# Performance work log

Measured on AMD Instinct MI355X. Metric: run time of the kernel, lower is better.

Reference implementation:

```python
import jax, jax.numpy as jnp
import numpy as np

B, P, D, K, OUT = 16, 2048, 64, 16, 128


def setup_inputs() -> dict:
    key = jax.random.key(0)
    k1, k2, k3 = jax.random.split(key, 3)
    x = jax.random.normal(k1, (B * P, D), dtype=jnp.float32)
    pos = jax.random.normal(k2, (B * P, 3), dtype=jnp.float32)
    batch = jnp.repeat(jnp.arange(B, dtype=jnp.int64), P)  # sorted segment ids
    # Linear(2*D -> OUT), torch convention W: [out, in]
    W = jax.random.normal(k3, (OUT, 2 * D), dtype=jnp.float32) / np.sqrt(2 * D)
    b = jnp.zeros((OUT,), dtype=jnp.float32)
    return {"x": x, "pos": pos, "batch": batch, "W": W, "b": b}


def _knn_idx(xb):
    # xb: [P, D] one cloud; returns [P, K] indices of K nearest neighbors (self excluded)
    sq = jnp.sum(xb * xb, axis=-1)  # [P]
    d2 = sq[:, None] + sq[None, :] - 2.0 * (xb @ xb.T)  # [P, P]
    d2 = d2 + jnp.eye(P, dtype=xb.dtype) * jnp.asarray(1e10, xb.dtype)  # loop=False
    _, idx = jax.lax.top_k(-d2, K)  # smallest distances
    return idx


def reference(x, pos, batch, W, b):
    # batch is uniform segments of size P (sorted), so reshape is equivalent
    xb = x.reshape(B, P, D)
    idx = jax.vmap(_knn_idx)(xb)  # [B, P, K]
    # gather neighbor features per cloud
    xj = jax.vmap(lambda f, i: f[i])(xb, idx)  # [B, P, K, D]
    xi = jnp.broadcast_to(xb[:, :, None, :], (B, P, K, D))
    e = jnp.concatenate([xi, xj - xi], axis=-1)  # [B, P, K, 2D]
    h = jnp.einsum('bpkd,od->bpko', e, W) + b  # edge MLP
    out = jnp.max(h, axis=2)  # max aggregation over neighbors -> [B, P, OUT]
    out = jax.nn.relu(out)
    return out.reshape(B * P, OUT)
```

## Files before the change

### kernel.cpp

```cpp
#include <hip/hip_runtime.h>

typedef __bf16 bf16x8 __attribute__((ext_vector_type(8)));
typedef float  f32x4  __attribute__((ext_vector_type(4)));

#define NBAT 16
#define NP   2048
#define ND   64
#define NOUT 128
#define NK   16
#define RT   16
#define HSTR 2052

static __device__ __forceinline__ unsigned short f2bf(float f) {
    unsigned u = __float_as_uint(f);
    u += 0x7FFF + ((u >> 16) & 1);
    return (unsigned short)(u >> 16);
}
static __device__ __forceinline__ int lanes_below(unsigned long long m) {
    return (int)__builtin_amdgcn_mbcnt_hi((unsigned)(m >> 32),
             __builtin_amdgcn_mbcnt_lo((unsigned)m, 0u));
}
static __device__ __forceinline__ unsigned long long umin64(unsigned long long a, unsigned long long b){ return a < b ? a : b; }
static __device__ __forceinline__ unsigned long long umax64(unsigned long long a, unsigned long long b){ return a < b ? b : a; }

static __device__ __forceinline__ void bitonic_sort128_u64(unsigned long long &k0,
                                                           unsigned long long &k1, int lane) {
#pragma unroll
    for (int k = 2; k <= 64; k <<= 1) {
#pragma unroll
        for (int j = k >> 1; j >= 1; j >>= 1) {
            bool lower = ((lane & j) == 0);
            bool up0 = (k == 64) ? true  : ((lane & k) == 0);
            bool up1 = (k == 64) ? false : ((lane & k) == 0);
            unsigned long long o0 = __shfl_xor(k0, j, 64);
            k0 = (up0 == lower) ? umin64(k0, o0) : umax64(k0, o0);
            unsigned long long o1 = __shfl_xor(k1, j, 64);
            k1 = (up1 == lower) ? umin64(k1, o1) : umax64(k1, o1);
        }
    }
    { unsigned long long mn = umin64(k0, k1), mx = umax64(k0, k1); k0 = mn; k1 = mx; }
#pragma unroll
    for (int j = 32; j >= 1; j >>= 1) {
        bool lower = ((lane & j) == 0);
        unsigned long long o0 = __shfl_xor(k0, j, 64);
        k0 = lower ? umin64(k0, o0) : umax64(k0, o0);
        unsigned long long o1 = __shfl_xor(k1, j, 64);
        k1 = lower ? umin64(k1, o1) : umax64(k1, o1);
    }
}

static __device__ __forceinline__ float
refine_d(const float* __restrict__ x, int gr, int gcbase, int jc) {
    const float* xr = x + (size_t)gr * ND;
    const float* xc = x + (size_t)(gcbase + jc) * ND;
    double s0 = 0.0, s1 = 0.0;
#pragma unroll
    for (int k8 = 0; k8 < 8; ++k8) {
        float4 a = *(const float4*)(xr + k8 * 8);
        float4 b = *(const float4*)(xc + k8 * 8);
        float4 a2 = *(const float4*)(xr + k8 * 8 + 4);
        float4 b2 = *(const float4*)(xc + k8 * 8 + 4);
        double e0 = (double)a.x - (double)b.x;
        double e1 = (double)a.y - (double)b.y;
        double e2 = (double)a.z - (double)b.z;
        double e3 = (double)a.w - (double)b.w;
        s0 = fma(e0, e0, s0); s0 = fma(e1, e1, s0);
        s0 = fma(e2, e2, s0); s0 = fma(e3, e3, s0);
        double f0 = (double)a2.x - (double)b2.x;
        double f1 = (double)a2.y - (double)b2.y;
        double f2 = (double)a2.z - (double)b2.z;
        double f3 = (double)a2.w - (double)b2.w;
        s1 = fma(f0, f0, s1); s1 = fma(f1, f1, s1);
        s1 = fma(f2, f2, s1); s1 = fma(f3, f3, s1);
    }
    return (float)(s0 + s1);
}

static __device__ __forceinline__ void cvt_hilo(const float* __restrict__ p,
                                                bf16x8 &hi, bf16x8 &lo) {
    float4 a = *(const float4*)p, b = *(const float4*)(p + 4);
    float f[8] = {a.x, a.y, a.z, a.w, b.x, b.y, b.z, b.w};
#pragma unroll
    for (int i = 0; i < 8; ++i) {
        __bf16 h = (__bf16)f[i];
        hi[i] = h;
        lo[i] = (__bf16)(f[i] - (float)h);
    }
}

__global__ void __launch_bounds__(256)
prep_k(const float* __restrict__ x,
       const float* __restrict__ W,
       const float* __restrict__ bias,
       float* __restrict__ sq, float* __restrict__ U,
       float* __restrict__ V,  unsigned short* __restrict__ xb16)
{
    const int blk = blockIdx.x, tid = threadIdx.x;
    const int R0 = blk * 16;
    const int w  = tid >> 6, l = tid & 63;
    const int l15 = l & 15, lg = l >> 4, kc = lg * 8;

    {
        int r = tid >> 4, c = (tid & 15) * 4;
        float4 v = *(const float4*)(x + (size_t)(R0 + r) * ND + c);
        ushort4 hb;
        hb.x = f2bf(v.x); hb.y = f2bf(v.y); hb.z = f2bf(v.z); hb.w = f2bf(v.w);
        *(ushort4*)(xb16 + (size_t)(R0 + r) * ND + c) = hb;
    }
    if (tid < 128) {
        int r = tid >> 3, seg = tid & 7;
        const float* p = x + (size_t)(R0 + r) * ND + seg * 8;
        float4 a = *(const float4*)(p);
        float4 b = *(const float4*)(p + 4);
        double s = (double)a.x * a.x + (double)a.y * a.y +
                   (double)a.z * a.z + (double)a.w * a.w +
                   (double)b.x * b.x + (double)b.y * b.y +
                   (double)b.z * b.z + (double)b.w * b.w;
        s += __shfl_xor(s, 1, 64);
        s += __shfl_xor(s, 2, 64);
        s += __shfl_xor(s, 4, 64);
        if (seg == 0) sq[R0 + r] = (float)s;
    }

    const float* xr = x + (size_t)(R0 + l15) * ND + kc;
    bf16x8 bh0, bl0, bh1, bl1;
    cvt_hilo(xr,      bh0, bl0);
    cvt_hilo(xr + 32, bh1, bl1);

#pragma unroll
    for (int tt = 0; tt < 2; ++tt) {
        const int ot = w + tt * 4;
        const float* wb = W + (size_t)(ot * 16 + l15) * (2 * ND) + kc;
        f32x4 accP = {0.f, 0.f, 0.f, 0.f};
        f32x4 accV = {0.f, 0.f, 0.f, 0.f};
        bf16x8 ah, al;
        cvt_hilo(wb, ah, al);
        accP = __builtin_amdgcn_mfma_f32_16x16x32_bf16(ah, bh0, accP, 0, 0, 0);
        accP = __builtin_amdgcn_mfma_f32_16x16x32_bf16(ah, bl0, accP, 0, 0, 0);
        accP = __builtin_amdgcn_mfma_f32_16x16x32_bf16(al, bh0, accP, 0, 0, 0);
        cvt_hilo(wb + 32, ah, al);
        accP = __builtin_amdgcn_mfma_f32_16x16x32_bf16(ah, bh1, accP, 0, 0, 0);
        accP = __builtin_amdgcn_mfma_f32_16x16x32_bf16(ah, bl1, accP, 0, 0, 0);
        accP = __builtin_amdgcn_mfma_f32_16x16x32_bf16(al, bh1, accP, 0, 0, 0);
        cvt_hilo(wb + 64, ah, al);
        accV = __builtin_amdgcn_mfma_f32_16x16x32_bf16(ah, bh0, accV, 0, 0, 0);
        accV = __builtin_amdgcn_mfma_f32_16x16x32_bf16(ah, bl0, accV, 0, 0, 0);
        accV = __builtin_amdgcn_mfma_f32_16x16x32_bf16(al, bh0, accV, 0, 0, 0);
        cvt_hilo(wb + 96, ah, al);
        accV = __builtin_amdgcn_mfma_f32_16x16x32_bf16(ah, bh1, accV, 0, 0, 0);
        accV = __builtin_amdgcn_mfma_f32_16x16x32_bf16(ah, bl1, accV, 0, 0, 0);
        accV = __builtin_amdgcn_mfma_f32_16x16x32_bf16(al, bh1, accV, 0, 0, 0);

        const int o0 = ot * 16 + lg * 4;
        float4 bo = *(const float4*)(bias + o0);
        float4 uu, vv;
        uu.x = accP[0] - accV[0] + bo.x;  vv.x = accV[0];
        uu.y = accP[1] - accV[1] + bo.y;  vv.y = accV[1];
        uu.z = accP[2] - accV[2] + bo.z;  vv.z = accV[2];
        uu.w = accP[3] - accV[3] + bo.w;  vv.w = accV[3];
        float* up = U + (size_t)(R0 + l15) * NOUT + o0;
        float* vp = V + (size_t)(R0 + l15) * NOUT + o0;
        *(float4*)up = uu;
        *(float4*)vp = vv;
    }
}

__global__ void __launch_bounds__(512, 2)
knn_k(const float* __restrict__ x,
      const unsigned short* __restrict__ xb16,
      const float* __restrict__ sq,
      const float* __restrict__ U,
      const float* __restrict__ V,
      float* __restrict__ out)
{
    extern __shared__ __align__(16) unsigned char smem[];
    unsigned short* d2h = (unsigned short*)smem;
    __shared__ unsigned short cbuf[8][128];

    const int q   = blockIdx.x;
    const int xcd = q & 7;
    const int k_  = q >> 3;
    const int bb  = xcd * 2 + (k_ >> 7);
    const int rt  = k_ & 127;
    const int R0l = rt * RT;
    const int R0g = bb * NP + R0l;
    const int tid = threadIdx.x;
    const int w   = tid >> 6;
    const int l   = tid & 63;
    const int l15 = l & 15, lg = l >> 4, kc = lg * 8;

    const unsigned short* nr = xb16 + (size_t)(R0g + l15) * ND + kc;
    bf16x8 n0 = *(const bf16x8*)(nr);
    bf16x8 n1 = *(const bf16x8*)(nr + 32);
    const float sqrow = sq[R0g + l15];

    const unsigned short* xbb = xb16 + (size_t)bb * NP * ND;
    const float* sqb = sq + bb * NP;

#pragma unroll 4
    for (int t = 0; t < 16; ++t) {
        const int cb = (w * 16 + t) * 16;
        const unsigned short* ar = xbb + (size_t)(cb + l15) * ND + kc;
        bf16x8 a0 = *(const bf16x8*)(ar);
        bf16x8 a1 = *(const bf16x8*)(ar + 32);
        f32x4 acc = {0.f, 0.f, 0.f, 0.f};
        acc = __builtin_amdgcn_mfma_f32_16x16x32_bf16(a0, n0, acc, 0, 0, 0);
        acc = __builtin_amdgcn_mfma_f32_16x16x32_bf16(a1, n1, acc, 0, 0, 0);
        const int jb4 = cb + lg * 4;
        float4 sq4 = *(const float4*)(sqb + jb4);
        unsigned short hh[4];
#pragma unroll
        for (int i = 0; i < 4; ++i) {
            float sqc = (i == 0) ? sq4.x : (i == 1) ? sq4.y : (i == 2) ? sq4.z : sq4.w;
            float d2 = fmaxf(fmaf(-2.f, acc[i], sqrow + sqc), 0.f);
            unsigned short h = __builtin_bit_cast(unsigned short, (_Float16)d2);
            if (R0l + l15 == jb4 + i) h = 0x7C00;
            hh[i] = h;
        }
        ushort4 hv; hv.x = hh[0]; hv.y = hh[1]; hv.z = hh[2]; hv.w = hh[3];
        *(ushort4*)(d2h + (size_t)l15 * HSTR + jb4) = hv;
    }
    __syncthreads();

    const int gcbase = bb * NP;
#pragma unroll 1
    for (int rr = 0; rr < 2; ++rr) {
        const int r  = w * 2 + rr;
        const int gr = R0g + r;
        const unsigned short* rowp = d2h + (size_t)r * HSTR;

        unsigned int h[32];
#pragma unroll
        for (int s = 0; s < 8; ++s) {
            ushort4 hv = *(const ushort4*)(rowp + (s * 64 + l) * 4);
            h[s*4+0] = hv.x; h[s*4+1] = hv.y; h[s*4+2] = hv.z; h[s*4+3] = hv.w;
        }
        unsigned int mnh = h[0];
#pragma unroll
        for (int i = 1; i < 32; ++i) mnh = (h[i] < mnh) ? h[i] : mnh;

        unsigned int t16 = 0;
#pragma unroll
        for (int b = 15; b >= 0; --b) {
            unsigned int cand = t16 | (1u << b);
            int c = __popcll(__ballot(mnh < cand));
            if (c < 16) t16 = cand;
        }
        float tf = (float)__builtin_bit_cast(_Float16, (unsigned short)t16) + 1.0f;
        unsigned int tauh =
            (unsigned int)__builtin_bit_cast(unsigned short, (_Float16)tf) + 1u;

        unsigned int packed = 0; int cnt = 0;
#pragma unroll
        for (int i = 0; i < 32; ++i) {
            if (h[i] <= tauh) {
                if (cnt < 4) packed |= (unsigned)i << (5 * cnt);
                ++cnt;
            }
        }
        bool ovf = (__ballot(cnt > 4) != 0ull);

        cbuf[w][l]      = 0xFFFF;
        cbuf[w][64 + l] = 0xFFFF;
        int total;
        if (!ovf) {
            int inc = cnt;
#pragma unroll
            for (int off = 1; off < 64; off <<= 1) {
                int nv = __shfl_up(inc, off, 64);
                if (l >= off) inc += nv;
            }
            int excl = inc - cnt;
            total = __shfl(inc, 63, 64);
#pragma unroll
            for (int kk = 0; kk < 4; ++kk) {
                if (kk < cnt && excl + kk < 128) {
                    int slot = (packed >> (5 * kk)) & 31;
                    cbuf[w][excl + kk] =
                        (unsigned short)(256 * (slot >> 2) + 4 * l + (slot & 3));
                }
            }
        } else {
            int base = 0;
#pragma unroll 1
            for (int i = 0; i < 32; ++i) {
                bool pred = (h[i] <= tauh);
                unsigned long long m = __ballot(pred);
                int pos = base + lanes_below(m);
                if (pred && pos < 128)
                    cbuf[w][pos] = (unsigned short)(256 * (i >> 2) + 4 * l + (i & 3));
                base += __popcll(m);
            }
            total = base;
        }
        asm volatile("s_waitcnt lgkmcnt(0)" ::: "memory");
        __builtin_amdgcn_sched_barrier(0);

        const float* Vb = V + (size_t)bb * NP * NOUT;
        float mv0 = -1e30f, mv1 = -1e30f;
        int jc = cbuf[w][l];

        bool fast = (total <= 64);
        unsigned long long win_m = 0ull;
        if (fast) {
            unsigned int dbits = 0xFFFFFFFFu;
            if (jc != 0xFFFF)
                dbits = __float_as_uint(refine_d(x, gr, gcbase, jc));

            unsigned int T = 0;
#pragma unroll
            for (int b = 30; b >= 0; --b) {
                unsigned int cand = T | (1u << b);
                int c = __popcll(__ballot(dbits < cand));
                if (c < 16) T = cand;
            }
            unsigned long long less_m = __ballot(dbits < T);
            int c_less = __popcll(less_m);
            int need = 16 - c_less;
            unsigned long long tie_m = __ballot(dbits == T);
            if (__popcll(tie_m) == need) {
                win_m = less_m | tie_m;
            } else {
                fast = false;
            }
        }

        if (fast) {
            int jns[NK];
            unsigned long long mm = win_m;
#pragma unroll
            for (int n = 0; n < NK; ++n) {
                int ln = __ffsll((long long)mm) - 1;
                jns[n] = __builtin_amdgcn_readlane(jc, ln);
                mm &= mm - 1;
            }
            float2 vv[NK];
#pragma unroll
            for (int n = 0; n < NK; ++n)
                vv[n] = *(const float2*)(Vb + (size_t)jns[n] * NOUT + (l << 1));
#pragma unroll
            for (int n = 0; n < NK; ++n) {
                mv0 = fmaxf(mv0, vv[n].x);
                mv1 = fmaxf(mv1, vv[n].y);
            }
        } else {
            int jc1 = cbuf[w][64 + l];
            unsigned long long rk0 = (jc != 0xFFFF)
                ? ((((unsigned long long)__float_as_uint(refine_d(x, gr, gcbase, jc))) << 11) | (unsigned)jc)
                : ~0ull;
            unsigned long long rk1 = (jc1 != 0xFFFF)
                ? ((((unsigned long long)__float_as_uint(refine_d(x, gr, gcbase, jc1))) << 11) | (unsigned)jc1)
                : ~0ull;
            bitonic_sort128_u64(rk0, rk1, l);
            int nbr = (int)(rk0 & 2047u);
            int jns[NK];
#pragma unroll
            for (int n = 0; n < NK; ++n)
                jns[n] = __builtin_amdgcn_readlane(nbr, n);
            float2 vv[NK];
#pragma unroll
            for (int n = 0; n < NK; ++n)
                vv[n] = *(const float2*)(Vb + (size_t)jns[n] * NOUT + (l << 1));
#pragma unroll
            for (int n = 0; n < NK; ++n) {
                mv0 = fmaxf(mv0, vv[n].x);
                mv1 = fmaxf(mv1, vv[n].y);
            }
        }

        float2 uu = *(const float2*)(U + (size_t)gr * NOUT + (l << 1));
        float2 ov;
        ov.x = fmaxf(uu.x + mv0, 0.f);
        ov.y = fmaxf(uu.y + mv1, 0.f);
        *(float2*)(out + (size_t)gr * NOUT + (l << 1)) = ov;
    }
}

extern "C" void kernel_launch(void* const* d_in, const int* in_sizes, int n_in,
                              void* d_out, int out_size, void* d_ws, size_t ws_size,
                              hipStream_t stream) {
    const float* x    = (const float*)d_in[0];
    const float* W    = (const float*)d_in[3];
    const float* bias = (const float*)d_in[4];
    float* out = (float*)d_out;

    float* sq = (float*)d_ws;
    float* U  = sq + NBAT * NP;
    float* V  = U  + (size_t)NBAT * NP * NOUT;
    unsigned short* xb16 = (unsigned short*)(V + (size_t)NBAT * NP * NOUT);

    prep_k<<<2048, 256, 0, stream>>>(x, W, bias, sq, U, V, xb16);

    const int lds_bytes = RT * HSTR * 2;
    (void)hipFuncSetAttribute((const void*)knn_k,
                        hipFuncAttributeMaxDynamicSharedMemorySize, lds_bytes);
    knn_k<<<2048, 512, lds_bytes, stream>>>(x, xb16, sq, U, V, out);
}
```

Baseline: 180.6 us.

## Amortize weight conversion in prep and use 16 waves per knn block

The prep kernel now processes 64 rows per block in four 16-row steps, converting the weight tile into hi/lo bf16 registers once and reusing it, so it launches a quarter as many blocks. The knn kernel doubles its block to 1024 threads so each wave computes half as many distance tiles and selects neighbors for one row instead of two, with the per-wave candidate buffer grown to 16 entries. This trades register pressure in prep and occupancy limits in knn for less redundant weight loading and more parallelism per row tile.

```diff
diff --git a/kernel.cpp b/kernel.cpp
--- a/kernel.cpp
+++ b/kernel.cpp
@@ -96,76 +96,85 @@
        float* __restrict__ V,  unsigned short* __restrict__ xb16)
 {
     const int blk = blockIdx.x, tid = threadIdx.x;
-    const int R0 = blk * 16;
+    const int R0b = blk * 64;
     const int w  = tid >> 6, l = tid & 63;
     const int l15 = l & 15, lg = l >> 4, kc = lg * 8;
 
-    {
-        int r = tid >> 4, c = (tid & 15) * 4;
-        float4 v = *(const float4*)(x + (size_t)(R0 + r) * ND + c);
-        ushort4 hb;
-        hb.x = f2bf(v.x); hb.y = f2bf(v.y); hb.z = f2bf(v.z); hb.w = f2bf(v.w);
-        *(ushort4*)(xb16 + (size_t)(R0 + r) * ND + c) = hb;
-    }
-    if (tid < 128) {
-        int r = tid >> 3, seg = tid & 7;
-        const float* p = x + (size_t)(R0 + r) * ND + seg * 8;
-        float4 a = *(const float4*)(p);
-        float4 b = *(const float4*)(p + 4);
-        double s = (double)a.x * a.x + (double)a.y * a.y +
-                   (double)a.z * a.z + (double)a.w * a.w +
-                   (double)b.x * b.x + (double)b.y * b.y +
-                   (double)b.z * b.z + (double)b.w * b.w;
-        s += __shfl_xor(s, 1, 64);
-        s += __shfl_xor(s, 2, 64);
-        s += __shfl_xor(s, 4, 64);
-        if (seg == 0) sq[R0 + r] = (float)s;
-    }
-
-    const float* xr = x + (size_t)(R0 + l15) * ND + kc;
-    bf16x8 bh0, bl0, bh1, bl1;
-    cvt_hilo(xr,      bh0, bl0);
-    cvt_hilo(xr + 32, bh1, bl1);
-
+    bf16x8 wh[2][4], wl[2][4];
 #pragma unroll
     for (int tt = 0; tt < 2; ++tt) {
-        const int ot = w + tt * 4;
-        const float* wb = W + (size_t)(ot * 16 + l15) * (2 * ND) + kc;
-        f32x4 accP = {0.f, 0.f, 0.f, 0.f};
-        f32x4 accV = {0.f, 0.f, 0.f, 0.f};
-        bf16x8 ah, al;
-        cvt_hilo(wb, ah, al);
-        accP = __builtin_amdgcn_mfma_f32_16x16x32_bf16(ah, bh0, accP, 0, 0, 0);
-        accP = __builtin_amdgcn_mfma_f32_16x16x32_bf16(ah, bl0, accP, 0, 0, 0);
-        accP = __builtin_amdgcn_mfma_f32_16x16x32_bf16(al, bh0, accP, 0, 0, 0);
-        cvt_hilo(wb + 32, ah, al);
-        accP = __builtin_amdgcn_mfma_f32_16x16x32_bf16(ah, bh1, accP, 0, 0, 0);
-        accP = __builtin_amdgcn_mfma_f32_16x16x32_bf16(ah, bl1, accP, 0, 0, 0);
-        accP = __builtin_amdgcn_mfma_f32_16x16x32_bf16(al, bh1, accP, 0, 0, 0);
-        cvt_hilo(wb + 64, ah, al);
-        accV = __builtin_amdgcn_mfma_f32_16x16x32_bf16(ah, bh0, accV, 0, 0, 0);
-        accV = __builtin_amdgcn_mfma_f32_16x16x32_bf16(ah, bl0, accV, 0, 0, 0);
-        accV = __builtin_amdgcn_mfma_f32_16x16x32_bf16(al, bh0, accV, 0, 0, 0);
-        cvt_hilo(wb + 96, ah, al);
-        accV = __builtin_amdgcn_mfma_f32_16x16x32_bf16(ah, bh1, accV, 0, 0, 0);
-        accV = __builtin_amdgcn_mfma_f32_16x16x32_bf16(ah, bl1, accV, 0, 0, 0);
-        accV = __builtin_amdgcn_mfma_f32_16x16x32_bf16(al, bh1, accV, 0, 0, 0);
-
-        const int o0 = ot * 16 + lg * 4;
-        float4 bo = *(const float4*)(bias + o0);
-        float4 uu, vv;
-        uu.x = accP[0] - accV[0] + bo.x;  vv.x = accV[0];
-        uu.y = accP[1] - accV[1] + bo.y;  vv.y = accV[1];
-        uu.z = accP[2] - accV[2] + bo.z;  vv.z = accV[2];
-        uu.w = accP[3] - accV[3] + bo.w;  vv.w = accV[3];
-        float* up = U + (size_t)(R0 + l15) * NOUT + o0;
-        float* vp = V + (size_t)(R0 + l15) * NOUT + o0;
-        *(float4*)up = uu;
-        *(float4*)vp = vv;
-    }
-}
-
-__global__ void __launch_bounds__(512, 2)
+        const float* wb = W + (size_t)((w + tt * 4) * 16 + l15) * (2 * ND) + kc;
+#pragma unroll
+        for (int p = 0; p < 4; ++p)
+            cvt_hilo(wb + p * 32, wh[tt][p], wl[tt][p]);
+    }
+    const int o0a = w * 16 + lg * 4;
+    const int o0b = (w + 4) * 16 + lg * 4;
+    float4 boa = *(const float4*)(bias + o0a);
+    float4 bob = *(const float4*)(bias + o0b);
+
+#pragma unroll 1
+    for (int s4 = 0; s4 < 4; ++s4) {
+        const int R0 = R0b + s4 * 16;
+
+        {
+            int r = tid >> 4, c = (tid & 15) * 4;
+            float4 v = *(const float4*)(x + (size_t)(R0 + r) * ND + c);
+            ushort4 hb;
+            hb.x = f2bf(v.x); hb.y = f2bf(v.y); hb.z = f2bf(v.z); hb.w = f2bf(v.w);
+            *(ushort4*)(xb16 + (size_t)(R0 + r) * ND + c) = hb;
+        }
+        if (tid < 128) {
+            int r = tid >> 3, seg = tid & 7;
+            const float* p = x + (size_t)(R0 + r) * ND + seg * 8;
+            float4 a = *(const float4*)(p);
+            float4 b = *(const float4*)(p + 4);
+            double s = (double)a.x * a.x + (double)a.y * a.y +
+                       (double)a.z * a.z + (double)a.w * a.w +
+                       (double)b.x * b.x + (double)b.y * b.y +
+                       (double)b.z * b.z + (double)b.w * b.w;
+            s += __shfl_xor(s, 1, 64);
+            s += __shfl_xor(s, 2, 64);
+            s += __shfl_xor(s, 4, 64);
+            if (seg == 0) sq[R0 + r] = (float)s;
+        }
+
+        const float* xr = x + (size_t)(R0 + l15) * ND + kc;
+        bf16x8 bh0, bl0, bh1, bl1;
+        cvt_hilo(xr,      bh0, bl0);
+        cvt_hilo(xr + 32, bh1, bl1);
+
+#pragma unroll
+        for (int tt = 0; tt < 2; ++tt) {
+            f32x4 accP = {0.f, 0.f, 0.f, 0.f};
+            f32x4 accV = {0.f, 0.f, 0.f, 0.f};
+            accP = __builtin_amdgcn_mfma_f32_16x16x32_bf16(wh[tt][0], bh0, accP, 0, 0, 0);
+            accP = __builtin_amdgcn_mfma_f32_16x16x32_bf16(wh[tt][0], bl0, accP, 0, 0, 0);
+            accP = __builtin_amdgcn_mfma_f32_16x16x32_bf16(wl[tt][0], bh0, accP, 0, 0, 0);
+            accP = __builtin_amdgcn_mfma_f32_16x16x32_bf16(wh[tt][1], bh1, accP, 0, 0, 0);
+            accP = __builtin_amdgcn_mfma_f32_16x16x32_bf16(wh[tt][1], bl1, accP, 0, 0, 0);
+            accP = __builtin_amdgcn_mfma_f32_16x16x32_bf16(wl[tt][1], bh1, accP, 0, 0, 0);
+            accV = __builtin_amdgcn_mfma_f32_16x16x32_bf16(wh[tt][2], bh0, accV, 0, 0, 0);
+            accV = __builtin_amdgcn_mfma_f32_16x16x32_bf16(wh[tt][2], bl0, accV, 0, 0, 0);
+            accV = __builtin_amdgcn_mfma_f32_16x16x32_bf16(wl[tt][2], bh0, accV, 0, 0, 0);
+            accV = __builtin_amdgcn_mfma_f32_16x16x32_bf16(wh[tt][3], bh1, accV, 0, 0, 0);
+            accV = __builtin_amdgcn_mfma_f32_16x16x32_bf16(wh[tt][3], bl1, accV, 0, 0, 0);
+            accV = __builtin_amdgcn_mfma_f32_16x16x32_bf16(wl[tt][3], bh1, accV, 0, 0, 0);
+
+            const int o0 = tt ? o0b : o0a;
+            float4 bo = tt ? bob : boa;
+            float4 uu, vv;
+            uu.x = accP[0] - accV[0] + bo.x;  vv.x = accV[0];
+            uu.y = accP[1] - accV[1] + bo.y;  vv.y = accV[1];
+            uu.z = accP[2] - accV[2] + bo.z;  vv.z = accV[2];
+            uu.w = accP[3] - accV[3] + bo.w;  vv.w = accV[3];
+            *(float4*)(U + (size_t)(R0 + l15) * NOUT + o0) = uu;
+            *(float4*)(V + (size_t)(R0 + l15) * NOUT + o0) = vv;
+        }
+    }
+}
+
+__global__ void __launch_bounds__(1024, 2)
 knn_k(const float* __restrict__ x,
       const unsigned short* __restrict__ xb16,
       const float* __restrict__ sq,
@@ -175,7 +184,7 @@
 {
     extern __shared__ __align__(16) unsigned char smem[];
     unsigned short* d2h = (unsigned short*)smem;
-    __shared__ unsigned short cbuf[8][128];
+    __shared__ unsigned short cbuf[16][128];
 
     const int q   = blockIdx.x;
     const int xcd = q & 7;
@@ -198,8 +207,8 @@
     const float* sqb = sq + bb * NP;
 
 #pragma unroll 4
-    for (int t = 0; t < 16; ++t) {
-        const int cb = (w * 16 + t) * 16;
+    for (int t = 0; t < 8; ++t) {
+        const int cb = (w * 8 + t) * 16;
         const unsigned short* ar = xbb + (size_t)(cb + l15) * ND + kc;
         bf16x8 a0 = *(const bf16x8*)(ar);
         bf16x8 a1 = *(const bf16x8*)(ar + 32);
@@ -223,9 +232,8 @@
     __syncthreads();
 
     const int gcbase = bb * NP;
-#pragma unroll 1
-    for (int rr = 0; rr < 2; ++rr) {
-        const int r  = w * 2 + rr;
+    {
+        const int r  = w;
         const int gr = R0g + r;
         const unsigned short* rowp = d2h + (size_t)r * HSTR;
 
@@ -389,10 +397,10 @@
     float* V  = U  + (size_t)NBAT * NP * NOUT;
     unsigned short* xb16 = (unsigned short*)(V + (size_t)NBAT * NP * NOUT);
 
-    prep_k<<<2048, 256, 0, stream>>>(x, W, bias, sq, U, V, xb16);
+    prep_k<<<512, 256, 0, stream>>>(x, W, bias, sq, U, V, xb16);
 
     const int lds_bytes = RT * HSTR * 2;
     (void)hipFuncSetAttribute((const void*)knn_k,
                         hipFuncAttributeMaxDynamicSharedMemorySize, lds_bytes);
-    knn_k<<<2048, 512, lds_bytes, stream>>>(x, xb16, sq, U, V, out);
-}
+    knn_k<<<2048, 1024, lds_bytes, stream>>>(x, xb16, sq, U, V, out);
+}
```

Result: faster. 159.5 us (-11.7%).
